# Performance work log

Hardware: AMD Instinct MI355X
Metric: run time of the kernel (lower is better)

## Reference

```python
import jax, jax.numpy as jnp
import numpy as np

L = 11
SF = 2
N, C, H, W = 8, 8, 256, 256


def _conv3(x, w, b):
    y = jax.lax.conv_general_dilated(x, w, (1, 1), ((1, 1), (1, 1)),
                                     dimension_numbers=('NCHW', 'OIHW', 'NCHW'))
    return y + b[None, :, None, None]


def _resblock(x, wa, ba, wb, bb):
    return _conv3(jax.nn.relu(_conv3(x, wa, ba)), wb, bb)


def _pronet(g, w1a, b1a, w1b, b1b, w2a, b2a, w2b, b2b, w3a, b3a, w3b, b3b,
            w4a, b4a, w4b, b4b, w5, b5):
    x1 = jax.nn.relu(g + 0.1 * _resblock(g, w1a, b1a, w1b, b1b))
    x2 = jax.nn.relu(x1 + 0.1 * _resblock(x1, w2a, b2a, w2b, b2b))
    x3 = jax.nn.relu(x2 + 0.1 * _resblock(x2, w3a, b3a, w3b, b3b))
    x4 = jax.nn.relu(x3 + 0.1 * _resblock(x3, w4a, b4a, w4b, b4b))
    return jax.nn.relu(g + 0.1 * _conv3(x4, w5, b5))


def _im2col(x, l, sf):
    # reflect-pad by (l-1)//2 then extract l x l patches with stride sf
    # -> [N, C, l*l, h*w], matching torch unfold's (c, kh, kw) channel order
    pad = (l - 1) // 2
    xp = jnp.pad(x, ((0, 0), (0, 0), (pad, pad), (pad, pad)), mode='reflect')
    n, c, hp, wp = xp.shape
    h = (hp - l) // sf + 1
    w = (wp - l) // sf + 1
    cols = [xp[:, :, i:i + (h - 1) * sf + 1:sf, j:j + (w - 1) * sf + 1:sf]
            for i in range(l) for j in range(l)]
    return jnp.stack(cols, axis=2).reshape(n, c, l * l, h * w), h, w


def setup_inputs() -> dict:
    key = jax.random.key(0)
    ks = jax.random.split(key, 22)
    h = (H - 1) // SF + 1
    inp = {
        'x': jax.random.normal(ks[0], (N, C, H, W), jnp.float32),
        'y': jax.random.normal(ks[1], (N, C, h, h), jnp.float32),
        'k': jax.random.uniform(ks[2], (N, C, L, L), jnp.float32),
        'sf': SF,
        'gamma': jnp.ones((), jnp.float32),
    }
    names = ['w1a', 'w1b', 'w2a', 'w2b', 'w3a', 'w3b', 'w4a', 'w4b', 'w5']
    for i, nm in enumerate(names):
        inp[nm] = 0.05 * jax.random.normal(ks[3 + i], (C, C, 3, 3), jnp.float32)
        inp['b' + nm[1:]] = 0.01 * jax.random.normal(ks[12 + i], (C,), jnp.float32)
    return inp


def reference(x, y, k, sf, gamma,
              w1a, b1a, w1b, b1b, w2a, b2a, w2b, b2b,
              w3a, b3a, w3b, b3b, w4a, b4a, w4b, b4b, w5, b5):
    n, c = x.shape[0], x.shape[1]
    l = k.shape[-1]
    x_col, h, w = _im2col(x, l, sf)                      # [N, C, l*l, h*w]
    kflat = k.reshape(n, c, l * l)
    # BatchBlur (grouped depthwise conv, groups=B*C) expressed as patch contraction
    blur = jnp.einsum('nckp,nck->ncp', x_col, kflat).reshape(n, c, h, w)
    # faithful torch .view: reinterpret [N,C,h,w] contiguous data as [N, h*w, C]
    R = (blur - y).reshape(n, h * w, c)
    # per-channel matmul loop fused into one batched contraction
    G = jnp.einsum('nckp,npc->nkc', x_col, R) / (h * w)  # [N, l*l, C]
    # faithful torch .view: reinterpret [N, l*l, C] as [N, C, l, l]
    G_K = k - (gamma / 10.0) * G.reshape(n, c, l, l)
    K = jax.nn.relu(_pronet(G_K, w1a, b1a, w1b, b1b, w2a, b2a, w2b, b2b,
                            w3a, b3a, w3b, b3b, w4a, b4a, w4b, b4b, w5, b5))
    return K / jnp.sum(K, axis=(2, 3), keepdims=True)
```

## Files before the change

kernel.cpp:

```cpp
#include <hip/hip_runtime.h>


__device__ __forceinline__ int refl(int m) {
    m = (m < 0) ? -m : m;
    return (m > 255) ? (510 - m) : m;
}

#define XPROW 272

__global__ __launch_bounds__(256) void pad_kernel(
        const float* __restrict__ x, float* __restrict__ xp) {
    int bid = blockIdx.x;
    int chunk = bid & 3;
    int nc = bid >> 2;
    int team = threadIdx.x >> 6;
    int lane = threadIdx.x & 63;
    const float* xb = x + nc * 65536;
    float* xpb = xp + nc * (256 * XPROW);
    for (int it = 0; it < 16; ++it) {
        int row = chunk * 64 + it * 4 + team;
        const float* src = xb + row * 256;
        float* dst = xpb + row * XPROW + 8;
        float4 v = reinterpret_cast<const float4*>(src)[lane];
        reinterpret_cast<float4*>(dst)[lane] = v;
        if (lane < 8) {
            dst[-1 - lane] = src[1 + lane];
        } else if (lane < 16) {
            int j = lane - 8;
            dst[256 + j] = src[254 - j];
        }
    }
}

__global__ __launch_bounds__(256) void blur_kernel(
        const float* __restrict__ xp, const float* __restrict__ y,
        const float* __restrict__ kk, float* __restrict__ E2) {
    __shared__ float kl[121];
    int bid = blockIdx.x;
    int rowblk = bid & 15;
    int nc = bid >> 4;
    int t = threadIdx.x;
    if (t < 121) kl[t] = kk[nc * 121 + t];
    __syncthreads();
    int r = rowblk * 8 + (t >> 5);
    int ps0 = (t & 31) * 4;
    const float* xb = xp + nc * (256 * XPROW);
    float a0 = 0.f, a1 = 0.f, a2 = 0.f, a3 = 0.f;
    #pragma unroll
    for (int i = 0; i < 11; ++i) {
        int iy = refl(2 * r - 5 + i);
        const float4* row4 = reinterpret_cast<const float4*>(xb + iy * XPROW + 2 * ps0);
        float w[24];
        #pragma unroll
        for (int q = 0; q < 6; ++q) {
            float4 v = row4[q];
            w[4 * q] = v.x; w[4 * q + 1] = v.y; w[4 * q + 2] = v.z; w[4 * q + 3] = v.w;
        }
        #pragma unroll
        for (int j = 0; j < 11; ++j) {
            float kv = kl[i * 11 + j];
            a0 = fmaf(w[j + 3], kv, a0);
            a1 = fmaf(w[j + 5], kv, a1);
            a2 = fmaf(w[j + 7], kv, a2);
            a3 = fmaf(w[j + 9], kv, a3);
        }
    }
    int n = nc >> 3;
    int o = nc * 16384 + r * 128 + ps0;
    float4 yv = *reinterpret_cast<const float4*>(y + o);
    float e[4] = {a0 - yv.x, a1 - yv.y, a2 - yv.z, a3 - yv.w};
    int qn = o - n * 131072;
    int p = qn >> 3;
    int cbase = qn & 7;
    float* eb = E2 + n * 131072 + p;
    #pragma unroll
    for (int qq = 0; qq < 4; ++qq)
        eb[(cbase + qq) * 16384] = e[qq];
}

__global__ __launch_bounds__(256) void grad_kernel(
        const float* __restrict__ xp, const float* __restrict__ E2,
        float* __restrict__ G) {
    int bid = blockIdx.x;
    int ki = bid % 11;
    int nc = bid / 11;
    int n = nc >> 3, c = nc & 7;
    const float* xb = xp + nc * (256 * XPROW);
    const float* Eb = E2 + n * 131072 + c * 16384;
    int t = threadIdx.x;
    int ps0 = (t & 31) * 4;
    int pr0 = t >> 5;
    float acc[11];
    #pragma unroll
    for (int j = 0; j < 11; ++j) acc[j] = 0.f;
    for (int it = 0; it < 16; ++it) {
        int pr = pr0 + (it << 3);
        int iy = refl(ki + 2 * pr - 5);
        float4 ev = *reinterpret_cast<const float4*>(Eb + pr * 128 + ps0);
        const float4* row4 = reinterpret_cast<const float4*>(xb + iy * XPROW + 2 * ps0);
        float w[24];
        #pragma unroll
        for (int q = 0; q < 6; ++q) {
            float4 v = row4[q];
            w[4 * q] = v.x; w[4 * q + 1] = v.y; w[4 * q + 2] = v.z; w[4 * q + 3] = v.w;
        }
        #pragma unroll
        for (int j = 0; j < 11; ++j) {
            float v = acc[j];
            v = fmaf(w[j + 3], ev.x, v);
            v = fmaf(w[j + 5], ev.y, v);
            v = fmaf(w[j + 7], ev.z, v);
            v = fmaf(w[j + 9], ev.w, v);
            acc[j] = v;
        }
    }
    __shared__ float part[4][11];
    int lane = t & 63, wid = t >> 6;
    #pragma unroll
    for (int j = 0; j < 11; ++j) {
        float v = acc[j];
        #pragma unroll
        for (int off = 32; off > 0; off >>= 1)
            v += __shfl_down(v, off, 64);
        if (lane == 0) part[wid][j] = v;
    }
    __syncthreads();
    if (t < 11) {
        float s = part[0][t] + part[1][t] + part[2][t] + part[3][t];
        G[n * 968 + (ki * 11 + t) * 8 + c] = s * (1.0f / 16384.0f);
    }
}

__global__ __launch_bounds__(256) void blur_kernel_ref(
        const float* __restrict__ x, const float* __restrict__ y,
        const float* __restrict__ kk, float* __restrict__ E2) {
    __shared__ float kl[121];
    int bid = blockIdx.x;
    int rowblk = bid & 15;
    int nc = bid >> 4;
    int t = threadIdx.x;
    if (t < 121) kl[t] = kk[nc * 121 + t];
    __syncthreads();
    int r = rowblk * 8 + (t >> 5);
    int ps0 = (t & 31) * 4;
    const float* xb = x + nc * 65536;
    float a0 = 0.f, a1 = 0.f, a2 = 0.f, a3 = 0.f;
    int cb = 2 * ps0 - 5;
    #pragma unroll
    for (int i = 0; i < 11; ++i) {
        int iy = refl(2 * r - 5 + i);
        const float* row = xb + iy * 256;
        float c[17];
        #pragma unroll
        for (int u = 0; u < 17; ++u) c[u] = row[refl(cb + u)];
        #pragma unroll
        for (int j = 0; j < 11; ++j) {
            float kv = kl[i * 11 + j];
            a0 = fmaf(c[j], kv, a0);
            a1 = fmaf(c[j + 2], kv, a1);
            a2 = fmaf(c[j + 4], kv, a2);
            a3 = fmaf(c[j + 6], kv, a3);
        }
    }
    int n = nc >> 3;
    int o = nc * 16384 + r * 128 + ps0;
    float4 yv = *reinterpret_cast<const float4*>(y + o);
    float e[4] = {a0 - yv.x, a1 - yv.y, a2 - yv.z, a3 - yv.w};
    int qn = o - n * 131072;
    int p = qn >> 3;
    int cbase = qn & 7;
    float* eb = E2 + n * 131072 + p;
    #pragma unroll
    for (int qq = 0; qq < 4; ++qq)
        eb[(cbase + qq) * 16384] = e[qq];
}

__global__ __launch_bounds__(256) void grad_kernel_ref(
        const float* __restrict__ x, const float* __restrict__ E2,
        float* __restrict__ G) {
    int bid = blockIdx.x;
    int ki = bid % 11;
    int nc = bid / 11;
    int n = nc >> 3, c = nc & 7;
    const float* xb = x + nc * 65536;
    const float* Eb = E2 + n * 131072 + c * 16384;
    int t = threadIdx.x;
    int ps0 = (t & 31) * 4;
    int pr0 = t >> 5;
    int cb = 2 * ps0 - 5;
    float acc[11];
    #pragma unroll
    for (int j = 0; j < 11; ++j) acc[j] = 0.f;
    for (int it = 0; it < 16; ++it) {
        int pr = pr0 + (it << 3);
        int iy = refl(ki + 2 * pr - 5);
        const float* row = xb + iy * 256;
        float cbuf[17];
        #pragma unroll
        for (int u = 0; u < 17; ++u) cbuf[u] = row[refl(cb + u)];
        float4 ev = *reinterpret_cast<const float4*>(Eb + pr * 128 + ps0);
        #pragma unroll
        for (int j = 0; j < 11; ++j) {
            float v = acc[j];
            v = fmaf(cbuf[j], ev.x, v);
            v = fmaf(cbuf[j + 2], ev.y, v);
            v = fmaf(cbuf[j + 4], ev.z, v);
            v = fmaf(cbuf[j + 6], ev.w, v);
            acc[j] = v;
        }
    }
    __shared__ float part[4][11];
    int lane = t & 63, wid = t >> 6;
    #pragma unroll
    for (int j = 0; j < 11; ++j) {
        float v = acc[j];
        #pragma unroll
        for (int off = 32; off > 0; off >>= 1)
            v += __shfl_down(v, off, 64);
        if (lane == 0) part[wid][j] = v;
    }
    __syncthreads();
    if (t < 11) {
        float s = part[0][t] + part[1][t] + part[2][t] + part[3][t];
        G[n * 968 + (ki * 11 + t) * 8 + c] = s * (1.0f / 16384.0f);
    }
}

struct PArgs {
    const float* W[9];
    const float* B[9];
    const float* k;
    const float* gamma;
    const float* G;
    float* out;
};

#define PLSTRIDE 20
#define WSTRIDE 12

__global__ __launch_bounds__(384) void pronet_kernel(PArgs pa) {
    __shared__ __align__(16) float P0[8 * 13 * PLSTRIDE];
    __shared__ __align__(16) float P1[8 * 13 * PLSTRIDE];
    __shared__ float G2[968];
    __shared__ float F[968];
    __shared__ __align__(16) float red[3 * 88 * WSTRIDE];
    __shared__ __align__(16) float wts[9 * 64 * WSTRIDE];
    __shared__ float bs[9 * 8];
    __shared__ float rowsum[88];
    __shared__ float inv[8];

    int n = blockIdx.x;
    int t = threadIdx.x;

    #pragma unroll
    for (int widx = 0; widx < 9; ++widx) {
        const float* wsrc = pa.W[widx];
        for (int i = t; i < 576; i += 384) {
            int oc = i / 9, q = i - oc * 9;
            wts[(widx * 64 + oc) * WSTRIDE + q] = wsrc[i];
        }
        if (t < 8) bs[widx * 8 + t] = pa.B[widx][t];
    }
    for (int i = t; i < 8 * 13 * PLSTRIDE; i += 384) { P0[i] = 0.f; P1[i] = 0.f; }
    __syncthreads();

    float gm = pa.gamma[0] * 0.1f;
    for (int o = t; o < 968; o += 384) {
        float v = pa.k[n * 968 + o] - gm * pa.G[n * 968 + o];
        G2[o] = v;
        int co = o / 121, rem = o - co * 121;
        int yy = rem / 11, xx = rem - yy * 11;
        P0[(co * 13 + yy + 1) * PLSTRIDE + xx + 1] = v;
    }

    bool active = t < 352;
    int quarter = t / 88;
    int id = t - quarter * 88;
    int co = id / 11, yy = id - co * 11;
    int ci0 = quarter * 2;

    auto do_conv = [&](const float* Pin, int widx, int mode) {
        __syncthreads();
        float acc[12];
        if (active) {
            #pragma unroll
            for (int xx = 0; xx < 12; ++xx) acc[xx] = 0.f;
            #pragma unroll
            for (int cq = 0; cq < 2; ++cq) {
                int ci = ci0 + cq;
                const float4* wp4 = reinterpret_cast<const float4*>(
                    &wts[(widx * 64 + co * 8 + ci) * WSTRIDE]);
                float4 w0 = wp4[0], w1 = wp4[1], w2 = wp4[2];
                float wv[9] = {w0.x, w0.y, w0.z, w0.w, w1.x, w1.y, w1.z, w1.w, w2.x};
                float r[3][13];
                #pragma unroll
                for (int dy = 0; dy < 3; ++dy) {
                    const float* row = Pin + (ci * 13 + yy + dy) * PLSTRIDE;
                    float4 a = *reinterpret_cast<const float4*>(row);
                    float4 b = *reinterpret_cast<const float4*>(row + 4);
                    float4 c = *reinterpret_cast<const float4*>(row + 8);
                    r[dy][0] = a.x;  r[dy][1] = a.y;  r[dy][2]  = a.z;  r[dy][3]  = a.w;
                    r[dy][4] = b.x;  r[dy][5] = b.y;  r[dy][6]  = b.z;  r[dy][7]  = b.w;
                    r[dy][8] = c.x;  r[dy][9] = c.y;  r[dy][10] = c.z;  r[dy][11] = c.w;
                    r[dy][12] = row[12];
                }
                #pragma unroll
                for (int xx = 0; xx < 11; ++xx) {
                    float v = acc[xx];
                    v = fmaf(r[0][xx],     wv[0], v);
                    v = fmaf(r[0][xx + 1], wv[1], v);
                    v = fmaf(r[0][xx + 2], wv[2], v);
                    v = fmaf(r[1][xx],     wv[3], v);
                    v = fmaf(r[1][xx + 1], wv[4], v);
                    v = fmaf(r[1][xx + 2], wv[5], v);
                    v = fmaf(r[2][xx],     wv[6], v);
                    v = fmaf(r[2][xx + 1], wv[7], v);
                    v = fmaf(r[2][xx + 2], wv[8], v);
                    acc[xx] = v;
                }
            }
            if (quarter != 0) {
                float4* rp = reinterpret_cast<float4*>(
                    &red[((quarter - 1) * 88 + id) * WSTRIDE]);
                rp[0] = make_float4(acc[0], acc[1], acc[2],  acc[3]);
                rp[1] = make_float4(acc[4], acc[5], acc[6],  acc[7]);
                rp[2] = make_float4(acc[8], acc[9], acc[10], acc[11]);
            }
        }
        __syncthreads();
        if (active && quarter == 0) {
            float b = bs[widx * 8 + co];
            float oth[12];
            #pragma unroll
            for (int pq = 0; pq < 3; ++pq) {
                const float4* rp = reinterpret_cast<const float4*>(
                    &red[(pq * 88 + id) * WSTRIDE]);
                float4 v0 = rp[0], v1 = rp[1], v2 = rp[2];
                if (pq == 0) {
                    oth[0] = v0.x; oth[1] = v0.y; oth[2]  = v0.z; oth[3]  = v0.w;
                    oth[4] = v1.x; oth[5] = v1.y; oth[6]  = v1.z; oth[7]  = v1.w;
                    oth[8] = v2.x; oth[9] = v2.y; oth[10] = v2.z; oth[11] = v2.w;
                } else {
                    oth[0] += v0.x; oth[1] += v0.y; oth[2]  += v0.z; oth[3]  += v0.w;
                    oth[4] += v1.x; oth[5] += v1.y; oth[6]  += v1.z; oth[7]  += v1.w;
                    oth[8] += v2.x; oth[9] += v2.y; oth[10] += v2.z; oth[11] += v2.w;
                }
            }
            #pragma unroll
            for (int xx = 0; xx < 11; ++xx) {
                float v = acc[xx] + oth[xx] + b;
                int pidx = (co * 13 + yy + 1) * PLSTRIDE + xx + 1;
                if (mode == 0) {
                    P1[pidx] = fmaxf(v, 0.f);
                } else if (mode == 1) {
                    float p = P0[pidx];
                    P0[pidx] = fmaxf(fmaf(0.1f, v, p), 0.f);
                } else {
                    int fo = co * 121 + yy * 11 + xx;
                    F[fo] = fmaxf(fmaf(0.1f, v, G2[fo]), 0.f);
                }
            }
        }
    };

    #pragma unroll
    for (int rb = 0; rb < 4; ++rb) {
        do_conv(P0, 2 * rb, 0);
        do_conv(P1, 2 * rb + 1, 1);
    }
    do_conv(P0, 8, 2);
    __syncthreads();

    if (t < 88) {
        int tco = t / 11, tyy = t - tco * 11;
        float s = 0.f;
        #pragma unroll
        for (int xx = 0; xx < 11; ++xx) s += F[tco * 121 + tyy * 11 + xx];
        rowsum[t] = s;
    }
    __syncthreads();
    if (t < 8) {
        float s = 0.f;
        #pragma unroll
        for (int j = 0; j < 11; ++j) s += rowsum[t * 11 + j];
        inv[t] = 1.f / s;
    }
    __syncthreads();
    for (int o = t; o < 968; o += 384)
        pa.out[n * 968 + o] = F[o] * inv[o / 121];
}

extern "C" void kernel_launch(void* const* d_in, const int* in_sizes, int n_in,
                              void* d_out, int out_size, void* d_ws, size_t ws_size,
                              hipStream_t stream) {
    const float* x = (const float*)d_in[0];
    const float* y = (const float*)d_in[1];
    const float* k = (const float*)d_in[2];
    const float* gamma = (const float*)d_in[4];

    const size_t xpad_fl = (size_t)64 * 256 * XPROW;
    const size_t e2_fl = (size_t)8 * 131072;
    const size_t need = (xpad_fl + e2_fl + 7744) * sizeof(float);

    float* G;
    if (ws_size >= need) {
        float* xpad = (float*)d_ws;
        float* E2 = xpad + xpad_fl;
        G = E2 + e2_fl;
        pad_kernel<<<256, 256, 0, stream>>>(x, xpad);
        blur_kernel<<<1024, 256, 0, stream>>>(xpad, y, k, E2);
        grad_kernel<<<704, 256, 0, stream>>>(xpad, E2, G);
    } else {
        float* E2 = (float*)d_ws;
        G = E2 + e2_fl;
        blur_kernel_ref<<<1024, 256, 0, stream>>>(x, y, k, E2);
        grad_kernel_ref<<<704, 256, 0, stream>>>(x, E2, G);
    }

    PArgs pa;
    for (int i = 0; i < 9; ++i) {
        pa.W[i] = (const float*)d_in[5 + 2 * i];
        pa.B[i] = (const float*)d_in[6 + 2 * i];
    }
    pa.k = k;
    pa.gamma = gamma;
    pa.G = G;
    pa.out = (float*)d_out;
    pronet_kernel<<<8, 384, 0, stream>>>(pa);
}
```

Baseline: 172.6 us.

## Fuse reflect-padding into blur kernel via shared-memory row tile and swizzle blocks

Merges the separate pad kernel into the blur kernel: each block loads its 25 input rows (with reflect halo) into shared memory, writes its 16 padded rows to the xpad buffer for the grad kernel, and computes the blur from shared memory instead of global padded rows. This removes one kernel launch and a full round trip of the padded image through global memory before blur. Block indices in both blur and grad kernels are also remapped with a stride-8 swizzle, likely to spread work across XCDs or improve cache locality. Costs about 27 KB of LDS per block, which may limit occupancy.

Result: slower. 177.4 us (+2.8%).

```diff
diff --git a/kernel.cpp b/kernel.cpp
--- a/kernel.cpp
+++ b/kernel.cpp
@@ -8,48 +8,49 @@
 
 #define XPROW 272
 
-__global__ __launch_bounds__(256) void pad_kernel(
-        const float* __restrict__ x, float* __restrict__ xp) {
+__global__ __launch_bounds__(256) void blur_fused_kernel(
+        const float* __restrict__ x, const float* __restrict__ y,
+        const float* __restrict__ kk, float* __restrict__ E2,
+        float* __restrict__ xp) {
+    __shared__ float kl[121];
+    __shared__ __align__(16) float S[25][XPROW];
     int bid = blockIdx.x;
-    int chunk = bid & 3;
-    int nc = bid >> 2;
-    int team = threadIdx.x >> 6;
-    int lane = threadIdx.x & 63;
+    int orig = ((bid & 7) << 7) | (bid >> 3);
+    int rowblk = orig & 15;
+    int nc = orig >> 4;
+    int t = threadIdx.x;
     const float* xb = x + nc * 65536;
+    if (t < 121) kl[t] = kk[nc * 121 + t];
+
+    int rowbase = 16 * rowblk - 5;
+    for (int i = t; i < 1600; i += 256) {
+        int s = i >> 6, c4 = i & 63;
+        int src = refl(rowbase + s);
+        float4 v = reinterpret_cast<const float4*>(xb + src * 256)[c4];
+        *reinterpret_cast<float4*>(&S[s][8 + 4 * c4]) = v;
+    }
+    if (t < 200) {
+        int s = t >> 3, u = t & 7;
+        const float* srow = xb + refl(rowbase + s) * 256;
+        S[s][7 - u]   = srow[1 + u];
+        S[s][264 + u] = srow[254 - u];
+    }
+    __syncthreads();
+
     float* xpb = xp + nc * (256 * XPROW);
-    for (int it = 0; it < 16; ++it) {
-        int row = chunk * 64 + it * 4 + team;
-        const float* src = xb + row * 256;
-        float* dst = xpb + row * XPROW + 8;
-        float4 v = reinterpret_cast<const float4*>(src)[lane];
-        reinterpret_cast<float4*>(dst)[lane] = v;
-        if (lane < 8) {
-            dst[-1 - lane] = src[1 + lane];
-        } else if (lane < 16) {
-            int j = lane - 8;
-            dst[256 + j] = src[254 - j];
-        }
-    }
-}
-
-__global__ __launch_bounds__(256) void blur_kernel(
-        const float* __restrict__ xp, const float* __restrict__ y,
-        const float* __restrict__ kk, float* __restrict__ E2) {
-    __shared__ float kl[121];
-    int bid = blockIdx.x;
-    int rowblk = bid & 15;
-    int nc = bid >> 4;
-    int t = threadIdx.x;
-    if (t < 121) kl[t] = kk[nc * 121 + t];
-    __syncthreads();
-    int r = rowblk * 8 + (t >> 5);
+    for (int i = t; i < 1088; i += 256) {
+        int rr = i / 68, c4 = i - rr * 68;
+        *reinterpret_cast<float4*>(&xpb[(16 * rowblk + rr) * XPROW + 4 * c4]) =
+            *reinterpret_cast<const float4*>(&S[rr + 5][4 * c4]);
+    }
+
+    int ty = t >> 5;
+    int r = rowblk * 8 + ty;
     int ps0 = (t & 31) * 4;
-    const float* xb = xp + nc * (256 * XPROW);
     float a0 = 0.f, a1 = 0.f, a2 = 0.f, a3 = 0.f;
     #pragma unroll
     for (int i = 0; i < 11; ++i) {
-        int iy = refl(2 * r - 5 + i);
-        const float4* row4 = reinterpret_cast<const float4*>(xb + iy * XPROW + 2 * ps0);
+        const float4* row4 = reinterpret_cast<const float4*>(&S[2 * ty + i][2 * ps0]);
         float w[24];
         #pragma unroll
         for (int q = 0; q < 6; ++q) {
@@ -82,8 +83,9 @@
         const float* __restrict__ xp, const float* __restrict__ E2,
         float* __restrict__ G) {
     int bid = blockIdx.x;
-    int ki = bid % 11;
-    int nc = bid / 11;
+    int orig = (bid & 7) * 88 + (bid >> 3);
+    int ki = orig % 11;
+    int nc = orig / 11;
     int n = nc >> 3, c = nc & 7;
     const float* xb = xp + nc * (256 * XPROW);
     const float* Eb = E2 + n * 131072 + c * 16384;
@@ -407,8 +409,7 @@
         float* xpad = (float*)d_ws;
         float* E2 = xpad + xpad_fl;
         G = E2 + e2_fl;
-        pad_kernel<<<256, 256, 0, stream>>>(x, xpad);
-        blur_kernel<<<1024, 256, 0, stream>>>(xpad, y, k, E2);
+        blur_fused_kernel<<<1024, 256, 0, stream>>>(x, y, k, E2, xpad);
         grad_kernel<<<704, 256, 0, stream>>>(xpad, E2, G);
     } else {
         float* E2 = (float*)d_ws;
```

## Swizzle block order across XCDs and widen pronet to one input channel per thread group

Applied to the files above, without the earlier changes.

Remaps block indices in the pad, blur and grad kernels so consecutive hardware block IDs spread across the eight XCDs while neighbouring logical work stays together per XCD, aiming at better L2 locality. The pronet kernel grows from 384 to 704 threads, giving each of eight 88-thread groups a single input channel instead of two. This halves the serial per-thread conv work but makes the shared-memory reduction sum seven partials. Weight loading is vectorised with float4. The latency-bound pronet stage gains parallelism at the cost of a larger reduction and more shared memory.

Measured after the change: 168.1 us. 2.6% less time.

```diff
diff --git a/kernel.cpp b/kernel.cpp
--- a/kernel.cpp
+++ b/kernel.cpp
@@ -11,8 +11,9 @@
 __global__ __launch_bounds__(256) void pad_kernel(
         const float* __restrict__ x, float* __restrict__ xp) {
     int bid = blockIdx.x;
-    int chunk = bid & 3;
-    int nc = bid >> 2;
+    int orig = (bid & 7) * 32 + (bid >> 3);
+    int chunk = orig & 3;
+    int nc = orig >> 2;
     int team = threadIdx.x >> 6;
     int lane = threadIdx.x & 63;
     const float* xb = x + nc * 65536;
@@ -37,8 +38,9 @@
         const float* __restrict__ kk, float* __restrict__ E2) {
     __shared__ float kl[121];
     int bid = blockIdx.x;
-    int rowblk = bid & 15;
-    int nc = bid >> 4;
+    int orig = ((bid & 7) << 7) | (bid >> 3);
+    int rowblk = orig & 15;
+    int nc = orig >> 4;
     int t = threadIdx.x;
     if (t < 121) kl[t] = kk[nc * 121 + t];
     __syncthreads();
@@ -82,8 +84,9 @@
         const float* __restrict__ xp, const float* __restrict__ E2,
         float* __restrict__ G) {
     int bid = blockIdx.x;
-    int ki = bid % 11;
-    int nc = bid / 11;
+    int orig = (bid & 7) * 88 + (bid >> 3);
+    int ki = orig % 11;
+    int nc = orig / 11;
     int n = nc >> 3, c = nc & 7;
     const float* xb = xp + nc * (256 * XPROW);
     const float* Eb = E2 + n * 131072 + c * 16384;
@@ -238,12 +241,12 @@
 #define PLSTRIDE 20
 #define WSTRIDE 12
 
-__global__ __launch_bounds__(384) void pronet_kernel(PArgs pa) {
+__global__ __launch_bounds__(704) void pronet_kernel(PArgs pa) {
     __shared__ __align__(16) float P0[8 * 13 * PLSTRIDE];
     __shared__ __align__(16) float P1[8 * 13 * PLSTRIDE];
     __shared__ float G2[968];
     __shared__ float F[968];
-    __shared__ __align__(16) float red[3 * 88 * WSTRIDE];
+    __shared__ __align__(16) float red[7 * 88 * WSTRIDE];
     __shared__ __align__(16) float wts[9 * 64 * WSTRIDE];
     __shared__ float bs[9 * 8];
     __shared__ float rowsum[88];
@@ -254,18 +257,24 @@
 
     #pragma unroll
     for (int widx = 0; widx < 9; ++widx) {
-        const float* wsrc = pa.W[widx];
-        for (int i = t; i < 576; i += 384) {
-            int oc = i / 9, q = i - oc * 9;
-            wts[(widx * 64 + oc) * WSTRIDE + q] = wsrc[i];
-        }
-        if (t < 8) bs[widx * 8 + t] = pa.B[widx][t];
-    }
-    for (int i = t; i < 8 * 13 * PLSTRIDE; i += 384) { P0[i] = 0.f; P1[i] = 0.f; }
+        if (t < 144) {
+            float4 v = reinterpret_cast<const float4*>(pa.W[widx])[t];
+            float vv[4] = {v.x, v.y, v.z, v.w};
+            #pragma unroll
+            for (int q2 = 0; q2 < 4; ++q2) {
+                int g = 4 * t + q2;
+                int oc = g / 9, q = g - oc * 9;
+                wts[(widx * 64 + oc) * WSTRIDE + q] = vv[q2];
+            }
+        } else if (t >= 640 && t < 648) {
+            bs[widx * 8 + (t - 640)] = pa.B[widx][t - 640];
+        }
+    }
+    for (int i = t; i < 8 * 13 * PLSTRIDE; i += 704) { P0[i] = 0.f; P1[i] = 0.f; }
     __syncthreads();
 
     float gm = pa.gamma[0] * 0.1f;
-    for (int o = t; o < 968; o += 384) {
+    for (int o = t; o < 968; o += 704) {
         float v = pa.k[n * 968 + o] - gm * pa.G[n * 968 + o];
         G2[o] = v;
         int co = o / 121, rem = o - co * 121;
@@ -273,66 +282,61 @@
         P0[(co * 13 + yy + 1) * PLSTRIDE + xx + 1] = v;
     }
 
-    bool active = t < 352;
-    int quarter = t / 88;
-    int id = t - quarter * 88;
+    int oct = t / 88;
+    int id = t - oct * 88;
     int co = id / 11, yy = id - co * 11;
-    int ci0 = quarter * 2;
+    int ci = oct;
 
     auto do_conv = [&](const float* Pin, int widx, int mode) {
         __syncthreads();
         float acc[12];
-        if (active) {
+        {
             #pragma unroll
             for (int xx = 0; xx < 12; ++xx) acc[xx] = 0.f;
-            #pragma unroll
-            for (int cq = 0; cq < 2; ++cq) {
-                int ci = ci0 + cq;
-                const float4* wp4 = reinterpret_cast<const float4*>(
-                    &wts[(widx * 64 + co * 8 + ci) * WSTRIDE]);
-                float4 w0 = wp4[0], w1 = wp4[1], w2 = wp4[2];
-                float wv[9] = {w0.x, w0.y, w0.z, w0.w, w1.x, w1.y, w1.z, w1.w, w2.x};
-                float r[3][13];
-                #pragma unroll
-                for (int dy = 0; dy < 3; ++dy) {
-                    const float* row = Pin + (ci * 13 + yy + dy) * PLSTRIDE;
-                    float4 a = *reinterpret_cast<const float4*>(row);
-                    float4 b = *reinterpret_cast<const float4*>(row + 4);
-                    float4 c = *reinterpret_cast<const float4*>(row + 8);
-                    r[dy][0] = a.x;  r[dy][1] = a.y;  r[dy][2]  = a.z;  r[dy][3]  = a.w;
-                    r[dy][4] = b.x;  r[dy][5] = b.y;  r[dy][6]  = b.z;  r[dy][7]  = b.w;
-                    r[dy][8] = c.x;  r[dy][9] = c.y;  r[dy][10] = c.z;  r[dy][11] = c.w;
-                    r[dy][12] = row[12];
-                }
-                #pragma unroll
-                for (int xx = 0; xx < 11; ++xx) {
-                    float v = acc[xx];
-                    v = fmaf(r[0][xx],     wv[0], v);
-                    v = fmaf(r[0][xx + 1], wv[1], v);
-                    v = fmaf(r[0][xx + 2], wv[2], v);
-                    v = fmaf(r[1][xx],     wv[3], v);
-                    v = fmaf(r[1][xx + 1], wv[4], v);
-                    v = fmaf(r[1][xx + 2], wv[5], v);
-                    v = fmaf(r[2][xx],     wv[6], v);
-                    v = fmaf(r[2][xx + 1], wv[7], v);
-                    v = fmaf(r[2][xx + 2], wv[8], v);
-                    acc[xx] = v;
-                }
-            }
-            if (quarter != 0) {
+            const float4* wp4 = reinterpret_cast<const float4*>(
+                &wts[(widx * 64 + co * 8 + ci) * WSTRIDE]);
+            float4 w0 = wp4[0], w1 = wp4[1], w2 = wp4[2];
+            float wv[9] = {w0.x, w0.y, w0.z, w0.w, w1.x, w1.y, w1.z, w1.w, w2.x};
+            float r[3][13];
+            #pragma unroll
+            for (int dy = 0; dy < 3; ++dy) {
+                const float* row = Pin + (ci * 13 + yy + dy) * PLSTRIDE;
+                float4 a = *reinterpret_cast<const float4*>(row);
+                float4 b = *reinterpret_cast<const float4*>(row + 4);
+                float4 c = *reinterpret_cast<const float4*>(row + 8);
+                r[dy][0] = a.x;  r[dy][1] = a.y;  r[dy][2]  = a.z;  r[dy][3]  = a.w;
+                r[dy][4] = b.x;  r[dy][5] = b.y;  r[dy][6]  = b.z;  r[dy][7]  = b.w;
+                r[dy][8] = c.x;  r[dy][9] = c.y;  r[dy][10] = c.z;  r[dy][11] = c.w;
+                r[dy][12] = row[12];
+            }
+            #pragma unroll
+            for (int xx = 0; xx < 11; ++xx) {
+                float v = acc[xx];
+                v = fmaf(r[0][xx],     wv[0], v);
+                v = fmaf(r[0][xx + 1], wv[1], v);
+                v = fmaf(r[0][xx + 2], wv[2], v);
+                v = fmaf(r[1][xx],     wv[3], v);
+                v = fmaf(r[1][xx + 1], wv[4], v);
+                v = fmaf(r[1][xx + 2], wv[5], v);
+                v = fmaf(r[2][xx],     wv[6], v);
+                v = fmaf(r[2][xx + 1], wv[7], v);
+                v = fmaf(r[2][xx + 2], wv[8], v);
+                acc[xx] = v;
+            }
+            if (oct != 0) {
                 float4* rp = reinterpret_cast<float4*>(
-                    &red[((quarter - 1) * 88 + id) * WSTRIDE]);
+                    &red[((oct - 1) * 88 + id) * WSTRIDE]);
                 rp[0] = make_float4(acc[0], acc[1], acc[2],  acc[3]);
                 rp[1] = make_float4(acc[4], acc[5], acc[6],  acc[7]);
                 rp[2] = make_float4(acc[8], acc[9], acc[10], acc[11]);
             }
         }
         __syncthreads();
-        if (active && quarter == 0) {
+        if (oct == 0) {
             float b = bs[widx * 8 + co];
             float oth[12];
             #pragma unroll
-            for (int pq = 0; pq < 3; ++pq) {
+            for (int pq = 0; pq < 7; ++pq) {
                 const float4* rp = reinterpret_cast<const float4*>(
                     &red[(pq * 88 + id) * WSTRIDE]);
                 float4 v0 = rp[0], v1 = rp[1], v2 = rp[2];
@@ -386,7 +390,7 @@
         inv[t] = 1.f / s;
     }
     __syncthreads();
-    for (int o = t; o < 968; o += 384)
+    for (int o = t; o < 968; o += 704)
         pa.out[n * 968 + o] = F[o] * inv[o / 121];
 }
 
@@ -426,5 +430,5 @@
     pa.gamma = gamma;
     pa.G = G;
     pa.out = (float*)d_out;
-    pronet_kernel<<<8, 384, 0, stream>>>(pa);
-}
+    pronet_kernel<<<8, 704, 0, stream>>>(pa);
+}
```
